# Optimization experiments

Hardware: AMD Instinct MI355X
Metric: run time of the kernel (lower is better)

Reference implementation:

```python
import jax, jax.numpy as jnp
import numpy as np

DIM = 1024
HEADS = 16
DIM_HEAD = 64
INNER = HEADS * DIM_HEAD
VID_LEN = 10
IMG_H, IMG_W = 16, 16
KS, KT = 5, 7  # kernel_spatial, kernel_temporal (causal=True)
BATCH = 1
SEQ = VID_LEN * IMG_H * IMG_W + 1  # +1 from causal pad -> 2561


def nearby_mask_causal(T, H, W, ks, kt):
    # numpy replication of generate_nearby_mask(causal=True); static, setup-time only
    te = (kt - 1) // 2
    frame = H * W
    S = T * frame
    p = ks // 2
    tmpl = (np.arange(ks * ks) >= (ks * ks) // 2).reshape(ks, ks)
    m = np.ones((S, T, H + 2 * p, W + 2 * p), dtype=bool)
    for t in range(T):
        for h in range(H):
            for w in range(W):
                i = t * frame + h * W + w
                m[i, t, h:h + ks, w:w + ks] = tmpl
                m[i, max(0, t - te):t, h:h + ks, w:w + ks] = False
    m = m[:, :, p:-p, p:-p].reshape(S, S)
    m = np.roll(m, -1, axis=0)
    m = np.pad(m, ((1, 0), (1, 0)), constant_values=True)
    m[0, 0] = False
    return m  # (S+1, S+1) bool; True = masked


def setup_inputs() -> dict:
    key = jax.random.key(0)
    ks = jax.random.split(key, 8)
    s = 0.02
    q = jax.random.normal(ks[0], (BATCH, SEQ, DIM), jnp.float32)
    k = jax.random.normal(ks[1], (BATCH, SEQ, DIM), jnp.float32)
    v = jax.random.normal(ks[2], (BATCH, SEQ, DIM), jnp.float32)
    Wq = jax.random.normal(ks[3], (DIM, INNER), jnp.float32) * s
    Wk = jax.random.normal(ks[4], (DIM, INNER), jnp.float32) * s
    Wv = jax.random.normal(ks[5], (DIM, INNER), jnp.float32) * s
    Wo = jax.random.normal(ks[6], (INNER, DIM), jnp.float32) * s
    bo = jnp.zeros((DIM,), jnp.float32)
    mask_block = jnp.asarray(nearby_mask_causal(VID_LEN, IMG_H, IMG_W, KS, KT))
    return {"q": q, "k": k, "v": v, "Wq": Wq, "Wk": Wk, "Wv": Wv,
            "Wo": Wo, "bo": bo, "mask_block": mask_block}


def reference(q, k, v, Wq, Wk, Wv, Wo, bo, mask_block):
    b, n, _ = q.shape
    h, dh = HEADS, DIM_HEAD
    scale = dh ** -0.5

    def heads_split(x, W):
        y = jnp.einsum('bnd,de->bne', x, W)
        return y.reshape(b, n, h, dh).transpose(0, 2, 1, 3)  # b h n dh

    qh = heads_split(q, Wq)
    kh = heads_split(k, Wk)
    vh = heads_split(v, Wv)
    dots = jnp.einsum('bhid,bhjd->bhij', qh, kh) * scale  # b h n n
    neg = -jnp.finfo(dots.dtype).max
    dots = jnp.where(mask_block[None, None], neg, dots)
    attn = jax.nn.softmax(dots, axis=-1)
    out = jnp.einsum('bhij,bhjd->bhid', attn, vh)
    out = out.transpose(0, 2, 1, 3).reshape(b, n, h * dh)
    out = jnp.einsum('bne,ed->bnd', out, Wo) + bo
    return out  # out[:, :n] is the identity here
```

## Files before the change

kernel.cpp:

```cpp
#include <hip/hip_runtime.h>
#include <float.h>

#define N_SEQ 2561
#define NPAD  2688
#define SEG   ((size_t)NPAD * 1024)
#define LOG2E 1.44269504088896340736f

typedef __attribute__((ext_vector_type(8))) short  short8;
typedef __attribute__((ext_vector_type(4))) short  s16x4;
typedef __attribute__((ext_vector_type(4))) float  f32x4;
typedef __attribute__((ext_vector_type(4))) unsigned int u32x4;
typedef __attribute__((ext_vector_type(4))) unsigned short u16x4;

__device__ __forceinline__ unsigned short f2bf(float f) {
  unsigned int u = __float_as_uint(f);
  u += 0x7FFFu + ((u >> 16) & 1u);
  return (unsigned short)(u >> 16);
}
__device__ __forceinline__ float bf2f(unsigned short v) {
  return __uint_as_float(((unsigned int)v) << 16);
}
__device__ __forceinline__ f32x4 mfma16(short8 a, short8 b, f32x4 c) {
  return __builtin_amdgcn_mfma_f32_16x16x32_bf16(a, b, c, 0, 0, 0);
}
__device__ __forceinline__ void load_lds16(const void* g, void* l) {
  __builtin_amdgcn_global_load_lds((const __attribute__((address_space(1))) void*)g,
                                   (__attribute__((address_space(3))) void*)l, 16, 0, 0);
}
__device__ __forceinline__ unsigned int cvt_pk_bf16(float a, float b) {
  unsigned int r;
  asm("v_cvt_pk_bf16_f32 %0, %1, %2" : "=v"(r) : "v"(a), "v"(b));
  return r;
}
__device__ __forceinline__ float fast_exp2(float x) {
  return __builtin_amdgcn_exp2f(x);
}

__global__ __launch_bounds__(256) void cvt_all(const float* __restrict__ q, const float* __restrict__ k,
                                               const float* __restrict__ v,
                                               const float* __restrict__ W0, const float* __restrict__ W1,
                                               const float* __restrict__ W2, const float* __restrict__ W3,
                                               unsigned short* __restrict__ Xq, unsigned short* __restrict__ Xk,
                                               unsigned short* __restrict__ Xv,
                                               unsigned short* __restrict__ T0, unsigned short* __restrict__ T1,
                                               unsigned short* __restrict__ T2, unsigned short* __restrict__ T3,
                                               uint2* __restrict__ Mtab) {
  __shared__ float tls[64][65];
  const int bid = blockIdx.x;
  if (bid < 4032) {
    const int by = bid / 1344, bx = bid - by * 1344;
    const float* src = (by == 0) ? q : (by == 1) ? k : v;
    unsigned short* dst = (by == 0) ? Xq : (by == 1) ? Xk : Xv;
    int idx = bx * 256 + threadIdx.x;
    size_t base = (size_t)idx * 8;
    int row = idx >> 7;
    short8 o;
    if (row < N_SEQ) {
      float4 a = *(const float4*)&src[base];
      float4 b = *(const float4*)&src[base + 4];
      o[0] = (short)f2bf(a.x); o[1] = (short)f2bf(a.y);
      o[2] = (short)f2bf(a.z); o[3] = (short)f2bf(a.w);
      o[4] = (short)f2bf(b.x); o[5] = (short)f2bf(b.y);
      o[6] = (short)f2bf(b.z); o[7] = (short)f2bf(b.w);
    } else {
      for (int j = 0; j < 8; ++j) o[j] = 0;
    }
    *(short8*)&dst[base] = o;
  } else if (bid < 5056) {
    const int b2 = bid - 4032;
    const int z = b2 >> 8, rem = b2 & 255;
    const int r0 = (rem >> 4) * 64, c0 = (rem & 15) * 64;
    const float* W; unsigned short* T; float scale = 1.0f;
    switch (z) {
      case 0: W = W0; T = T0; scale = 0.125f * LOG2E; break;
      case 1: W = W1; T = T1; break;
      case 2: W = W2; T = T2; break;
      default: W = W3; T = T3; break;
    }
    const int tid = threadIdx.x, tr = tid >> 4, tc = tid & 15;
#pragma unroll
    for (int u = 0; u < 4; ++u) {
      int row = tr + u * 16;
      float4 vv = *(const float4*)&W[(size_t)(r0 + row) * 1024 + c0 + tc * 4];
      tls[tc * 4 + 0][row] = vv.x; tls[tc * 4 + 1][row] = vv.y;
      tls[tc * 4 + 2][row] = vv.z; tls[tc * 4 + 3][row] = vv.w;
    }
    __syncthreads();
#pragma unroll
    for (int u = 0; u < 4; ++u) {
      int crow = tr + u * 16;
      u16x4 o;
#pragma unroll
      for (int j = 0; j < 4; ++j) o[j] = f2bf(tls[crow][tc * 4 + j] * scale);
      *(u16x4*)&T[(size_t)(c0 + crow) * 1024 + r0 + tc * 4] = o;
    }
  } else {
    const int idx = (bid - 5056) * 256 + threadIdx.x;
    const int r = idx >> 6, lane = idx & 63;
    const int lhi = lane >> 4, llo = lane & 15;
    const int rlo5 = min(max(r - 2, 0), 11);
    unsigned mpast = 0, mcur = 0;
#pragma unroll
    for (int n = 0; n < 6; ++n)
#pragma unroll
      for (int rr = 0; rr < 4; ++rr) {
        int s = n * 16 + lhi * 4 + rr;
        int u = rlo5 * 16 + s - 1;
        if (u < 0 || u > 255) continue;
        int rk = u >> 4, ck = u & 15;
        int dr = rk - r, dc = ck - llo;
        if (dr < -2 || dr > 2 || dc < -2 || dc > 2) continue;
        mpast |= 1u << (n * 4 + rr);
        if (dr < 0 || (dr == 0 && dc < 0)) mcur |= 1u << (n * 4 + rr);
      }
    Mtab[idx] = make_uint2(mpast, mcur);
  }
}

__device__ __forceinline__ void stage_tile(const unsigned short* A, const unsigned short* Bt,
                                           unsigned short* Asm, unsigned short* Bsm,
                                           int i0, int c0, int k0, int w, int srow, int scol) {
#pragma unroll
  for (int u = 0; u < 4; ++u) {
    int row = w * 32 + u * 8 + srow;
    load_lds16(&A [(size_t)(i0 + row) * 1024 + k0 + scol], &Asm[(w * 32 + u * 8) * 64]);
    load_lds16(&Bt[(size_t)(c0 + row) * 1024 + k0 + scol], &Bsm[(w * 32 + u * 8) * 64]);
  }
}

template <int MODE>
__device__ __forceinline__ void gemm_core(const unsigned short* A, const unsigned short* Bt,
                                          unsigned short* C, int i0, int c0,
                                          unsigned short* Asm, unsigned short* Bsm) {
  const int tid = threadIdx.x, w = tid >> 6, lane = tid & 63;
  const int wr = w >> 1, wc = w & 1;
  const int srow = lane >> 3;
  const int scol = ((lane & 7) * 8) ^ (srow << 3);
  f32x4 acc[4][4] = {};

  stage_tile(A, Bt, Asm, Bsm, i0, c0, 0, w, srow, scol);

  for (int t = 0; t < 16; ++t) {
    __syncthreads();
    if (t < 15)
      stage_tile(A, Bt, Asm + ((t + 1) & 1) * 8192, Bsm + ((t + 1) & 1) * 8192,
                 i0, c0, (t + 1) * 64, w, srow, scol);
    const unsigned short* Ab = Asm + (t & 1) * 8192;
    const unsigned short* Bb = Bsm + (t & 1) * 8192;
#pragma unroll
    for (int kk = 0; kk < 2; ++kk) {
      const int colel = kk * 32 + (lane >> 4) * 8;
      short8 af[4], bf[4];
#pragma unroll
      for (int m = 0; m < 4; ++m) {
        int row = wr * 64 + m * 16 + (lane & 15);
        af[m] = *(const short8*)&Ab[row * 64 + (colel ^ ((row & 7) << 3))];
      }
#pragma unroll
      for (int n = 0; n < 4; ++n) {
        int row = wc * 64 + n * 16 + (lane & 15);
        bf[n] = *(const short8*)&Bb[row * 64 + (colel ^ ((row & 7) << 3))];
      }
#pragma unroll
      for (int m = 0; m < 4; ++m)
#pragma unroll
        for (int n = 0; n < 4; ++n)
          acc[m][n] = mfma16(af[m], bf[n], acc[m][n]);
    }
  }

#pragma unroll
  for (int m = 0; m < 4; ++m)
#pragma unroll
    for (int n = 0; n < 4; ++n) {
      const int col = c0 + wc * 64 + n * 16 + (lane & 15);
#pragma unroll
      for (int r = 0; r < 4; ++r) {
        const int row = i0 + wr * 64 + m * 16 + (lane >> 4) * 4 + r;
        if (MODE == 1) {
          C[((size_t)(col >> 6) * NPAD + row) * 64 + (col & 63)] = f2bf(acc[m][n][r]);
        } else {
          C[(((size_t)(row >> 6) * 168 + (col >> 4)) * 64 + (row & 63)) * 16 + (col & 15)] = f2bf(acc[m][n][r]);
        }
      }
    }
}

__global__ __launch_bounds__(256) void proj3(const unsigned short* __restrict__ Xq, const unsigned short* __restrict__ WqT, unsigned short* __restrict__ Qh,
                                             const unsigned short* __restrict__ Xk, const unsigned short* __restrict__ WkT, unsigned short* __restrict__ Kh,
                                             const unsigned short* __restrict__ WvT, const unsigned short* __restrict__ Xv, unsigned short* __restrict__ Vt) {
  __shared__ unsigned short Asm[2 * 8192];
  __shared__ unsigned short Bsm[2 * 8192];
  int b = blockIdx.x;
  b = (b & 7) * 63 + (b >> 3);
  if (b < 168) {
    int r = b;
    gemm_core<1>(Xq, WqT, Qh, (r >> 3) * 128, (r & 7) * 128, Asm, Bsm);
  } else if (b < 336) {
    int r = b - 168;
    gemm_core<1>(Xk, WkT, Kh, (r >> 3) * 128, (r & 7) * 128, Asm, Bsm);
  } else {
    int r = b - 336;
    gemm_core<2>(WvT, Xv, Vt, (r / 21) * 128, (r % 21) * 128, Asm, Bsm);
  }
}

__global__ __launch_bounds__(256) void outproj(const unsigned short* __restrict__ A, const unsigned short* __restrict__ Bt,
                                               float* __restrict__ out, const float* __restrict__ bias) {
  __shared__ unsigned short Asm[2 * 4096];
  __shared__ unsigned short Bsm[2 * 8192];
  int b = (blockIdx.x & 7) * 42 + (blockIdx.x >> 3);
  const int i0 = (b >> 3) * 64, c0 = (b & 7) * 128;
  const int tid = threadIdx.x, w = tid >> 6, lane = tid & 63;
  const int wr = w >> 1, wc = w & 1;
  const int srow = lane >> 3;
  const int scol = ((lane & 7) * 8) ^ (srow << 3);
  const int llo = lane & 15, lhi = lane >> 4;
  f32x4 acc[2][4] = {};

#define STAGE64(buf, k0)                                                                     \
  {                                                                                          \
    _Pragma("unroll")                                                                        \
    for (int u = 0; u < 2; ++u) {                                                            \
      int row = w * 16 + u * 8 + srow;                                                       \
      load_lds16(&A[(size_t)(i0 + row) * 1024 + (k0) + scol], &Asm[(buf) * 4096 + (w * 16 + u * 8) * 64]); \
    }                                                                                        \
    _Pragma("unroll")                                                                        \
    for (int u = 0; u < 4; ++u) {                                                            \
      int row = w * 32 + u * 8 + srow;                                                       \
      load_lds16(&Bt[(size_t)(c0 + row) * 1024 + (k0) + scol], &Bsm[(buf) * 8192 + (w * 32 + u * 8) * 64]); \
    }                                                                                        \
  }

  STAGE64(0, 0)
  for (int t = 0; t < 16; ++t) {
    __syncthreads();
    if (t < 15) STAGE64((t + 1) & 1, (t + 1) * 64)
    const unsigned short* Ab = Asm + (t & 1) * 4096;
    const unsigned short* Bb = Bsm + (t & 1) * 8192;
#pragma unroll
    for (int kk = 0; kk < 2; ++kk) {
      const int colel = kk * 32 + lhi * 8;
      short8 af[2], bf[4];
#pragma unroll
      for (int m = 0; m < 2; ++m) {
        int row = wr * 32 + m * 16 + llo;
        af[m] = *(const short8*)&Ab[row * 64 + (colel ^ ((row & 7) << 3))];
      }
#pragma unroll
      for (int n = 0; n < 4; ++n) {
        int row = wc * 64 + n * 16 + llo;
        bf[n] = *(const short8*)&Bb[row * 64 + (colel ^ ((row & 7) << 3))];
      }
#pragma unroll
      for (int m = 0; m < 2; ++m)
#pragma unroll
        for (int n = 0; n < 4; ++n)
          acc[m][n] = mfma16(af[m], bf[n], acc[m][n]);
    }
  }
#undef STAGE64

#pragma unroll
  for (int m = 0; m < 2; ++m)
#pragma unroll
    for (int n = 0; n < 4; ++n) {
      const int col = c0 + wc * 64 + n * 16 + llo;
      const float bb = bias[col];
#pragma unroll
      for (int r = 0; r < 4; ++r) {
        const int row = i0 + wr * 32 + m * 16 + lhi * 4 + r;
        if (row < N_SEQ) out[(size_t)row * 1024 + col] = acc[m][n][r] + bb;
      }
    }
}

__global__ __launch_bounds__(256, 3) void attn_span6(const unsigned short* __restrict__ Qh,
                                                     const unsigned short* __restrict__ Kh,
                                                     const unsigned short* __restrict__ Vt,
                                                     unsigned short* __restrict__ Ob,
                                                     const uint2* __restrict__ Mtab) {
  __shared__ float Lacc[3][64][17];
  __shared__ float Ll[4][16];
  int bid = blockIdx.x + blockIdx.y * 160;
  bid = (bid & 7) * 320 + (bid >> 3);
  const int qg = bid % 160, h = bid / 160;
  const int w = threadIdx.x >> 6, lane = threadIdx.x & 63;
  const int lhi = lane >> 4, llo = lane & 15;
  const int t = qg >> 4, r = qg & 15;
  const int rlo5 = min(max(r - 2, 0), 11);
  const int f = t - 3 + w;

  const uint2 mm = Mtab[(r << 6) + lane];
  const unsigned msk = (w == 3) ? mm.y : mm.x;

  f32x4 acc[4] = {};
  float l = 0.f;

  if (f >= 0) {
    const int jb0 = f * 256 + rlo5 * 16;

    const unsigned short* qp = &Qh[((size_t)h * NPAD + qg * 16 + llo) * 64 + lhi * 8];
    short8 qf0 = *(const short8*)&qp[0];
    short8 qf1 = *(const short8*)&qp[32];

    short8 kf[6][2];
    const unsigned short* kbase = &Kh[((size_t)h * NPAD + jb0) * 64];
#pragma unroll
    for (int n = 0; n < 6; ++n) {
      const unsigned short* kp = kbase + (n * 16 + llo) * 64;
      kf[n][0] = *(const short8*)&kp[lhi * 8];
      kf[n][1] = *(const short8*)&kp[32 + lhi * 8];
    }
    s16x4 vv[3][4][2];
    const size_t tb = (size_t)h * 168 + (jb0 >> 4);
#pragma unroll
    for (int kk = 0; kk < 3; ++kk)
#pragma unroll
      for (int n2 = 0; n2 < 4; ++n2) {
        vv[kk][n2][0] = *(const s16x4*)&Vt[((tb + kk * 2)     * 64 + n2 * 16 + llo) * 16 + lhi * 4];
        vv[kk][n2][1] = *(const s16x4*)&Vt[((tb + kk * 2 + 1) * 64 + n2 * 16 + llo) * 16 + lhi * 4];
      }
    __builtin_amdgcn_sched_barrier(0);
    asm volatile("" ::: "memory");

    __builtin_amdgcn_s_setprio(1);
    float p[6][4];
#pragma unroll
    for (int n = 0; n < 6; ++n) {
      f32x4 z = {0.f, 0.f, 0.f, 0.f};
      z = mfma16(kf[n][0], qf0, z);
      z = mfma16(kf[n][1], qf1, z);
#pragma unroll
      for (int rr = 0; rr < 4; ++rr) {
        float pv = ((msk >> (n * 4 + rr)) & 1u) ? fast_exp2(z[rr]) : 0.f;
        p[n][rr] = pv;
        l += pv;
      }
    }

#pragma unroll
    for (int kk = 0; kk < 3; ++kk) {
      const int n0 = kk * 2;
      u32x4 pw;
      pw[0] = cvt_pk_bf16(p[n0][0], p[n0][1]);
      pw[1] = cvt_pk_bf16(p[n0][2], p[n0][3]);
      pw[2] = cvt_pk_bf16(p[n0 + 1][0], p[n0 + 1][1]);
      pw[3] = cvt_pk_bf16(p[n0 + 1][2], p[n0 + 1][3]);
      short8 pf = __builtin_bit_cast(short8, pw);
#pragma unroll
      for (int n2 = 0; n2 < 4; ++n2) {
        short8 vf = __builtin_shufflevector(vv[kk][n2][0], vv[kk][n2][1], 0, 1, 2, 3, 4, 5, 6, 7);
        acc[n2] = mfma16(pf, vf, acc[n2]);
      }
    }
    __builtin_amdgcn_s_setprio(0);
  }

  l += __shfl_xor(l, 16);
  l += __shfl_xor(l, 32);
  if (lhi == 0) Ll[w][llo] = l;
  if (w > 0) {
#pragma unroll
    for (int n2 = 0; n2 < 4; ++n2)
#pragma unroll
      for (int rr = 0; rr < 4; ++rr)
        Lacc[w - 1][lane][n2 * 4 + rr] = acc[n2][rr];
  }
  __syncthreads();
  if (w == 0) {
    const float lt = Ll[0][llo] + Ll[1][llo] + Ll[2][llo] + Ll[3][llo];
    float li[4];
#pragma unroll
    for (int rr = 0; rr < 4; ++rr) li[rr] = 1.0f / __shfl(lt, lhi * 4 + rr);
#pragma unroll
    for (int rr = 0; rr < 4; ++rr) {
      const int row = qg * 16 + lhi * 4 + rr;
#pragma unroll
      for (int n2 = 0; n2 < 4; ++n2) {
        float s = acc[n2][rr] + Lacc[0][lane][n2 * 4 + rr]
                              + Lacc[1][lane][n2 * 4 + rr]
                              + Lacc[2][lane][n2 * 4 + rr];
        Ob[(size_t)row * 1024 + h * 64 + n2 * 16 + llo] = f2bf(s * li[rr]);
      }
    }
  }
}

__global__ void fix_rows(const unsigned short* __restrict__ Vt, unsigned short* __restrict__ Ob) {
  const int d = blockIdx.x, lane = threadIdx.x;
  const int h = d >> 6, dd = d & 63;
  const int kb4 = lane >> 4, ks = lane & 15;
  float s = 0.f;
  for (int kb = kb4; kb < 168; kb += 4)
    s += bf2f(Vt[(((size_t)h * 168 + kb) * 64 + dd) * 16 + ks]);
  s += __shfl_xor(s, 1);  s += __shfl_xor(s, 2);  s += __shfl_xor(s, 4);
  s += __shfl_xor(s, 8);  s += __shfl_xor(s, 16); s += __shfl_xor(s, 32);
  if (lane == 0) {
    Ob[(size_t)2560 * 1024 + d] = f2bf(s * (1.0f / 2561.0f));
    Ob[d] = Vt[((size_t)h * 168 * 64 + dd) * 16];
  }
}

extern "C" void kernel_launch(void* const* d_in, const int* in_sizes, int n_in,
                              void* d_out, int out_size, void* d_ws, size_t ws_size,
                              hipStream_t stream) {
  const float* q  = (const float*)d_in[0];
  const float* k  = (const float*)d_in[1];
  const float* v  = (const float*)d_in[2];
  const float* Wq = (const float*)d_in[3];
  const float* Wk = (const float*)d_in[4];
  const float* Wv = (const float*)d_in[5];
  const float* Wo = (const float*)d_in[6];
  const float* bo = (const float*)d_in[7];

  unsigned short* ws = (unsigned short*)d_ws;
  const size_t MW = (size_t)1024 * 1024;
  unsigned short* Xq  = ws;
  unsigned short* Xk  = ws + SEG;
  unsigned short* Xv  = ws + 2 * SEG;
  unsigned short* Qh  = ws + 3 * SEG;
  unsigned short* Kh  = ws + 4 * SEG;
  unsigned short* Vt  = ws + 5 * SEG;
  unsigned short* WqT = ws + 6 * SEG;
  unsigned short* WkT = WqT + MW;
  unsigned short* WvT = WqT + 2 * MW;
  unsigned short* WoT = WqT + 3 * MW;
  uint2* Mtab = (uint2*)(WqT + 4 * MW);
  unsigned short* ObB = Xq;

  cvt_all<<<5060, 256, 0, stream>>>(q, k, v, Wq, Wk, Wv, Wo, Xq, Xk, Xv, WqT, WkT, WvT, WoT, Mtab);

  proj3<<<504, 256, 0, stream>>>(Xq, WqT, Qh, Xk, WkT, Kh, WvT, Xv, Vt);

  attn_span6<<<dim3(160, 16), 256, 0, stream>>>(Qh, Kh, Vt, ObB, Mtab);
  fix_rows<<<1024, 64, 0, stream>>>(Vt, ObB);

  outproj<<<336, 256, 0, stream>>>(ObB, WoT, (float*)d_out, bo);
}
```

Baseline: 96.13 us.

## Fold row-fix kernel into attention grid and shrink outproj tiles

The separate fix_rows kernel is removed. Its work (the V column mean for the last row and the copy for row 0) now runs in an extra block column of the attention grid, and the attention epilogue skips writing row 0 to avoid a race. The output projection tile goes from 64x128 to 64x64, doubling the block count to 672 for better CU occupancy on the small GEMM. This drops one launch, at the cost of more redundant A-tile loads in outproj.

```diff
diff --git a/kernel.cpp b/kernel.cpp
--- a/kernel.cpp
+++ b/kernel.cpp
@@ -208,15 +208,15 @@
 __global__ __launch_bounds__(256) void outproj(const unsigned short* __restrict__ A, const unsigned short* __restrict__ Bt,
                                                float* __restrict__ out, const float* __restrict__ bias) {
   __shared__ unsigned short Asm[2 * 4096];
-  __shared__ unsigned short Bsm[2 * 8192];
-  int b = (blockIdx.x & 7) * 42 + (blockIdx.x >> 3);
-  const int i0 = (b >> 3) * 64, c0 = (b & 7) * 128;
+  __shared__ unsigned short Bsm[2 * 4096];
+  int b = (blockIdx.x & 7) * 84 + (blockIdx.x >> 3);
+  const int i0 = (b >> 4) * 64, c0 = (b & 15) * 64;
   const int tid = threadIdx.x, w = tid >> 6, lane = tid & 63;
   const int wr = w >> 1, wc = w & 1;
   const int srow = lane >> 3;
   const int scol = ((lane & 7) * 8) ^ (srow << 3);
   const int llo = lane & 15, lhi = lane >> 4;
-  f32x4 acc[2][4] = {};
+  f32x4 acc[2][2] = {};
 
 #define STAGE64(buf, k0)                                                                     \
   {                                                                                          \
@@ -224,11 +224,7 @@
     for (int u = 0; u < 2; ++u) {                                                            \
       int row = w * 16 + u * 8 + srow;                                                       \
       load_lds16(&A[(size_t)(i0 + row) * 1024 + (k0) + scol], &Asm[(buf) * 4096 + (w * 16 + u * 8) * 64]); \
-    }                                                                                        \
-    _Pragma("unroll")                                                                        \
-    for (int u = 0; u < 4; ++u) {                                                            \
-      int row = w * 32 + u * 8 + srow;                                                       \
-      load_lds16(&Bt[(size_t)(c0 + row) * 1024 + (k0) + scol], &Bsm[(buf) * 8192 + (w * 32 + u * 8) * 64]); \
+      load_lds16(&Bt[(size_t)(c0 + row) * 1024 + (k0) + scol], &Bsm[(buf) * 4096 + (w * 16 + u * 8) * 64]); \
     }                                                                                        \
   }
 
@@ -237,25 +233,25 @@
     __syncthreads();
     if (t < 15) STAGE64((t + 1) & 1, (t + 1) * 64)
     const unsigned short* Ab = Asm + (t & 1) * 4096;
-    const unsigned short* Bb = Bsm + (t & 1) * 8192;
+    const unsigned short* Bb = Bsm + (t & 1) * 4096;
 #pragma unroll
     for (int kk = 0; kk < 2; ++kk) {
       const int colel = kk * 32 + lhi * 8;
-      short8 af[2], bf[4];
+      short8 af[2], bf[2];
 #pragma unroll
       for (int m = 0; m < 2; ++m) {
         int row = wr * 32 + m * 16 + llo;
         af[m] = *(const short8*)&Ab[row * 64 + (colel ^ ((row & 7) << 3))];
       }
 #pragma unroll
-      for (int n = 0; n < 4; ++n) {
-        int row = wc * 64 + n * 16 + llo;
+      for (int n = 0; n < 2; ++n) {
+        int row = wc * 32 + n * 16 + llo;
         bf[n] = *(const short8*)&Bb[row * 64 + (colel ^ ((row & 7) << 3))];
       }
 #pragma unroll
       for (int m = 0; m < 2; ++m)
 #pragma unroll
-        for (int n = 0; n < 4; ++n)
+        for (int n = 0; n < 2; ++n)
           acc[m][n] = mfma16(af[m], bf[n], acc[m][n]);
     }
   }
@@ -264,8 +260,8 @@
 #pragma unroll
   for (int m = 0; m < 2; ++m)
 #pragma unroll
-    for (int n = 0; n < 4; ++n) {
-      const int col = c0 + wc * 64 + n * 16 + llo;
+    for (int n = 0; n < 2; ++n) {
+      const int col = c0 + wc * 32 + n * 16 + llo;
       const float bb = bias[col];
 #pragma unroll
       for (int r = 0; r < 4; ++r) {
@@ -282,6 +278,31 @@
                                                      const uint2* __restrict__ Mtab) {
   __shared__ float Lacc[3][64][17];
   __shared__ float Ll[4][16];
+
+  if (blockIdx.x == 160) {
+    __shared__ float part[4][64];
+    const int h = blockIdx.y;
+    const int tid = threadIdx.x;
+    const int dd = tid & 63, p = tid >> 6;
+    float s = 0.f;
+    for (int kb = p; kb < 168; kb += 4) {
+      const unsigned short* vp = &Vt[(((size_t)h * 168 + kb) * 64 + dd) * 16];
+      short8 a = *(const short8*)&vp[0];
+      short8 bq = *(const short8*)&vp[8];
+#pragma unroll
+      for (int j = 0; j < 8; ++j)
+        s += bf2f((unsigned short)a[j]) + bf2f((unsigned short)bq[j]);
+    }
+    part[p][dd] = s;
+    __syncthreads();
+    if (p == 0) {
+      float tot = part[0][dd] + part[1][dd] + part[2][dd] + part[3][dd];
+      Ob[(size_t)2560 * 1024 + h * 64 + dd] = f2bf(tot * (1.0f / 2561.0f));
+      Ob[h * 64 + dd] = Vt[(((size_t)h * 168) * 64 + dd) * 16];
+    }
+    return;
+  }
+
   int bid = blockIdx.x + blockIdx.y * 160;
   bid = (bid & 7) * 320 + (bid >> 3);
   const int qg = bid % 160, h = bid / 160;
@@ -376,6 +397,7 @@
 #pragma unroll
     for (int rr = 0; rr < 4; ++rr) {
       const int row = qg * 16 + lhi * 4 + rr;
+      if (row == 0) continue;
 #pragma unroll
       for (int n2 = 0; n2 < 4; ++n2) {
         float s = acc[n2][rr] + Lacc[0][lane][n2 * 4 + rr]
@@ -384,21 +406,6 @@
         Ob[(size_t)row * 1024 + h * 64 + n2 * 16 + llo] = f2bf(s * li[rr]);
       }
     }
-  }
-}
-
-__global__ void fix_rows(const unsigned short* __restrict__ Vt, unsigned short* __restrict__ Ob) {
-  const int d = blockIdx.x, lane = threadIdx.x;
-  const int h = d >> 6, dd = d & 63;
-  const int kb4 = lane >> 4, ks = lane & 15;
-  float s = 0.f;
-  for (int kb = kb4; kb < 168; kb += 4)
-    s += bf2f(Vt[(((size_t)h * 168 + kb) * 64 + dd) * 16 + ks]);
-  s += __shfl_xor(s, 1);  s += __shfl_xor(s, 2);  s += __shfl_xor(s, 4);
-  s += __shfl_xor(s, 8);  s += __shfl_xor(s, 16); s += __shfl_xor(s, 32);
-  if (lane == 0) {
-    Ob[(size_t)2560 * 1024 + d] = f2bf(s * (1.0f / 2561.0f));
-    Ob[d] = Vt[((size_t)h * 168 * 64 + dd) * 16];
   }
 }
 
@@ -433,8 +440,7 @@
 
   proj3<<<504, 256, 0, stream>>>(Xq, WqT, Qh, Xk, WkT, Kh, WvT, Xv, Vt);
 
-  attn_span6<<<dim3(160, 16), 256, 0, stream>>>(Qh, Kh, Vt, ObB, Mtab);
-  fix_rows<<<1024, 64, 0, stream>>>(Vt, ObB);
-
-  outproj<<<336, 256, 0, stream>>>(ObB, WoT, (float*)d_out, bo);
-}
+  attn_span6<<<dim3(161, 16), 256, 0, stream>>>(Qh, Kh, Vt, ObB, Mtab);
+
+  outproj<<<672, 256, 0, stream>>>(ObB, WoT, (float*)d_out, bo);
+}
```

New measurement: 88.78 us, median of 2. 1.08x faster.
